# Kernel tuning notes

Measured on AMD Instinct MI355X. Metric: run time of the kernel, lower is better.

Reference implementation:

```python
import jax, jax.numpy as jnp
from jax import lax
import numpy as np

BATCH, SEQ, N, M, U = 256, 4096, 16, 8, 4  # batch, seq_len, state, obs, input dims


def setup_inputs() -> dict:
    key = jax.random.key(0)
    ks = jax.random.split(key, 8)
    # stable transition matrix (spectral radius < 1)
    A_raw = jax.random.normal(ks[0], (N, N), dtype=jnp.float32)
    A = 0.9 * A_raw / jnp.linalg.norm(A_raw, ord=2)
    B = jax.random.normal(ks[1], (N, U), dtype=jnp.float32) * 0.1
    C = jax.random.normal(ks[2], (M, N), dtype=jnp.float32) * 0.3
    # SPD noise covariances
    Q = 0.01 * jnp.eye(N, dtype=jnp.float32)
    R = 0.1 * jnp.eye(M, dtype=jnp.float32)
    obs = jax.random.normal(ks[3], (BATCH, SEQ, M), dtype=jnp.float32)
    inputs = jax.random.normal(ks[4], (BATCH, SEQ, U), dtype=jnp.float32)
    x0 = jax.random.normal(ks[5], (N,), dtype=jnp.float32)
    return {"obs": obs, "inputs": inputs, "A": A, "B": B, "C": C, "Q": Q, "R": R, "x0": x0}


def _kalman(obs, inputs, A, B, C, Q, R, x0):
    n = A.shape[0]
    bsz = obs.shape[0]
    eye_n = jnp.eye(n, dtype=obs.dtype)

    def step(carry, zu):
        x, P = carry              # x: (B, n), P: (n, n) shared across batch
        z, u = zu                 # z: (B, m), u: (B, u)
        # stage 1: state prediction
        x_pri = x @ A.T + u @ B.T               # (B, n)
        P_pri = A @ P @ A.T + Q                 # (n, n)
        # stage 2: measurement update
        S = C @ P_pri @ C.T + R                 # (m, m)
        K = P_pri @ C.T @ jnp.linalg.inv(S)     # (n, m)
        innov = z - x_pri @ C.T                 # (B, m)
        x_post = x_pri + innov @ K.T            # (B, n)
        P_post = (eye_n - K @ C) @ P_pri        # (n, n)
        return (x_post, P_post), x_post

    x_init = jnp.broadcast_to(x0, (bsz, n))
    zs = jnp.swapaxes(obs[:, 1:, :], 0, 1)      # (T-1, B, m)
    us = jnp.swapaxes(inputs[:, 1:, :], 0, 1)   # (T-1, B, u)
    _, xs = lax.scan(step, (x_init, eye_n), (zs, us))
    states = jnp.concatenate([x_init[:, None, :], jnp.swapaxes(xs, 0, 1)], axis=1)
    return states                                # (B, T, n)


def reference(obs, inputs, A, B, C, Q, R, x0):
    return _kalman(obs, inputs, A, B, C, Q, R, x0)
```

## Files before the change

### kernel.cpp

```cpp
#include <hip/hip_runtime.h>


#define SEQ_T  4096
#define NSTEP  4095
#define NB     256
#define NEX    8
#define LCH    32
#define NCHT   128

#define EX_OFF 0
#define ST_OFF (NEX*448)
#define HI_OFF (ST_OFF+448)
#define DB_OFF (HI_OFF+256)

template<int KQ>
__device__ __forceinline__ void bc4(const float* xr, float* xk) {
#pragma unroll
  for (int r = 0; r < 4; r++)
    xk[r] = __int_as_float(__builtin_amdgcn_update_dpp(
        0, __float_as_int(xr[r]), KQ * 0x55, 0xF, 0xF, true));
}

__global__ __launch_bounds__(64) void k_riccati(
    const float* __restrict__ Ag, const float* __restrict__ Bg,
    const float* __restrict__ Cg, const float* __restrict__ Qg,
    const float* __restrict__ Rg, float* __restrict__ ws)
{
  const int l = threadIdx.x;
  __shared__ float As[256], Qs[256], Cs[128], Bs[64], CA[128], CB[32];
  __shared__ float Pp[256], Vv[128], Km[128], Gm[256], T1[256], T2[256], Xs[64];

#pragma unroll
  for (int j=0;j<4;j++){ int e=l+64*j; As[e]=Ag[e]; Qs[e]=Qg[e]; }
  Cs[l]=Cg[l]; Cs[l+64]=Cg[l+64];
  Bs[l]=Bg[l];
  const float rr = Rg[l];
  __syncthreads();

  const int r4=l>>2, g4=l&3;
  const int r8=l>>3, c8=l&7;

  { int e=l; { int r=e>>4,c=e&15; float a=0.f;
      for (int k=0;k<16;k++) a+=Cs[r*16+k]*As[k*16+c]; CA[e]=a; }
    e=l+64; { int r=e>>4,c=e&15; float a=0.f;
      for (int k=0;k<16;k++) a+=Cs[r*16+k]*As[k*16+c]; CA[e]=a; }
    if (l<32){ int r=l>>2,c=l&3; float a=0.f;
      for (int k=0;k<16;k++) a+=Cs[r*16+k]*Bs[k*4+c]; CB[l]=a; }
#pragma unroll
    for (int j=0;j<4;j++){ int c=4*g4+j; float a=Qs[r4*16+c];
      for (int k=0;k<16;k++) a+=As[r4*16+k]*As[c*16+k]; Pp[r4*16+c]=a; }
  }
  __syncthreads();

  float kv0=0.f, kv1=0.f, bfv=0.f;
  for (int s=0;s<NEX;s++){
    { int e=l; { int r=e>>3,c=e&7; float a=0.f;
        for (int k=0;k<16;k++) a+=Pp[r*16+k]*Cs[c*16+k]; Vv[e]=a; }
      e=l+64; { int r=e>>3,c=e&7; float a=0.f;
        for (int k=0;k<16;k++) a+=Pp[r*16+k]*Cs[c*16+k]; Vv[e]=a; } }
    __syncthreads();
    { float sv=rr;
      for (int k=0;k<16;k++) sv += Cs[r8*16+k]*Vv[k*8+c8];
      float xv = (r8==c8)?1.f:0.f;
#pragma unroll
      for (int p=0;p<8;p++){
        float spp = __shfl(sv, p*9);
        float pr  = 1.0f/spp;
        float spc = __shfl(sv, p*8+c8);
        float xpc = __shfl(xv, p*8+c8);
        float srp = __shfl(sv, r8*8+p);
        float f = srp*pr;
        if (r8==p){ sv = spc*pr; xv = xpc*pr; }
        else      { sv -= f*spc; xv -= f*xpc; }
      }
      Xs[l]=xv; }
    __syncthreads();
    { int e=l; { int r=e>>3,c=e&7; float a=0.f;
        for (int k=0;k<8;k++) a+=Vv[r*8+k]*Xs[k*8+c]; kv0=a; Km[e]=a; }
      e=l+64; { int r=e>>3,c=e&7; float a=0.f;
        for (int k=0;k<8;k++) a+=Vv[r*8+k]*Xs[k*8+c]; kv1=a; Km[e]=a; } }
    __syncthreads();
    { float gv[4];
#pragma unroll
      for (int j=0;j<4;j++){ int c=4*g4+j;
        float a=As[r4*16+c], w=Pp[r4*16+c];
        for (int k=0;k<8;k++){ a -= Km[r4*8+k]*CA[k*16+c]; w -= Km[r4*8+k]*Vv[c*8+k]; }
        gv[j]=a; Gm[r4*16+c]=a; Pp[r4*16+c]=w; }
      bfv = Bs[l];
      for (int k=0;k<8;k++) bfv -= Km[r4*8+k]*CB[k*4+g4];
      float* dst = ws + EX_OFF + s*448;
      *reinterpret_cast<float4*>(dst + r4*16 + g4*4) =
          make_float4(gv[0],gv[1],gv[2],gv[3]);
      dst[256+l]=kv0; dst[256+64+l]=kv1; dst[384+l]=bfv;
    }
    __syncthreads();
#pragma unroll
    for (int j=0;j<4;j++){ int c=4*g4+j; float a=0.f;
      for (int k=0;k<16;k++) a+=As[r4*16+k]*Pp[k*16+c]; T1[r4*16+c]=a; }
    __syncthreads();
#pragma unroll
    for (int j=0;j<4;j++){ int c=4*g4+j; float a=Qs[r4*16+c];
      for (int k=0;k<16;k++) a+=T1[r4*16+k]*As[c*16+k]; Pp[r4*16+c]=a; }
    __syncthreads();
  }
  { float* dst = ws + ST_OFF;
    *reinterpret_cast<float4*>(dst + r4*16 + g4*4) =
        *reinterpret_cast<float4*>(&Gm[r4*16 + g4*4]);
    dst[256+l]=kv0; dst[256+64+l]=kv1; dst[384+l]=bfv; }
#pragma unroll
  for (int j=0;j<4;j++) T1[l+64*j]=Gm[l+64*j];
  __syncthreads();
  for (int it=0; it<5; it++){
#pragma unroll
    for (int j=0;j<4;j++){ int c=4*g4+j; float a=0.f;
      for (int k=0;k<16;k++) a+=T1[r4*16+k]*T1[k*16+c]; T2[r4*16+c]=a; }
    __syncthreads();
#pragma unroll
    for (int j=0;j<4;j++) T1[l+64*j]=T2[l+64*j];
    __syncthreads();
  }
#pragma unroll
  for (int j=0;j<4;j++) ws[HI_OFF + l+64*j] = T1[l+64*j];
}

__device__ __forceinline__ void ld_rows(const float* __restrict__ m, int q,
    float gm[4][16], float km[4][8], float bf[4][4]) {
#pragma unroll
  for (int r=0;r<4;r++){
    const int row = 4*q + r;
    const float4* gp = reinterpret_cast<const float4*>(m + row*16);
#pragma unroll
    for (int kk=0;kk<4;kk++){ float4 t=gp[kk];
      gm[r][4*kk]=t.x; gm[r][4*kk+1]=t.y; gm[r][4*kk+2]=t.z; gm[r][4*kk+3]=t.w; }
    const float4* kp = reinterpret_cast<const float4*>(m + 256 + row*8);
#pragma unroll
    for (int kk=0;kk<2;kk++){ float4 t=kp[kk];
      km[r][4*kk]=t.x; km[r][4*kk+1]=t.y; km[r][4*kk+2]=t.z; km[r][4*kk+3]=t.w; }
    float4 t = *reinterpret_cast<const float4*>(m + 384 + row*4);
    bf[r][0]=t.x; bf[r][1]=t.y; bf[r][2]=t.z; bf[r][3]=t.w;
  }
}

template<int MODE>
__device__ __forceinline__ void chunk_run(
    const float* __restrict__ obs, const float* __restrict__ inp,
    const float* __restrict__ x0g, float* __restrict__ ws,
    float* __restrict__ out, int j, int g)
{
  const int l=threadIdx.x, bl=l>>2, q=l&3, b=g*16+bl;
  const int s0 = j*LCH;
  const int nst = (NSTEP - s0 < LCH) ? (NSTEP - s0) : LCH;

  float gm[4][16], km[4][8], bf[4][4];
  if (MODE==1) ld_rows(ws + EX_OFF, q, gm, km, bf);
  else         ld_rows(ws + ST_OFF, q, gm, km, bf);

  float xr[4];
  if (MODE==0){ xr[0]=xr[1]=xr[2]=xr[3]=0.f; }
  else if (MODE==1){
    float4 x = *reinterpret_cast<const float4*>(x0g + q*4);
    xr[0]=x.x; xr[1]=x.y; xr[2]=x.z; xr[3]=x.w;
    *reinterpret_cast<float4*>(out + (size_t)b*(SEQ_T*16) + q*4) = x;
  } else {
    float4 x = *reinterpret_cast<const float4*>(
        ws + DB_OFF + (size_t)(j-1)*(NB*16) + b*16 + q*4);
    xr[0]=x.x; xr[1]=x.y; xr[2]=x.z; xr[3]=x.w;
  }

  const float* zp = obs + (size_t)b*(SEQ_T*8);
  const float* up = inp + (size_t)b*(SEQ_T*4);

  float4 z0a = *reinterpret_cast<const float4*>(zp + (size_t)(s0+1)*8);
  float4 z1a = *reinterpret_cast<const float4*>(zp + (size_t)(s0+1)*8 + 4);
  float4 u0a = *reinterpret_cast<const float4*>(up + (size_t)(s0+1)*4);
  float4 z0b = *reinterpret_cast<const float4*>(zp + (size_t)(s0+2)*8);
  float4 z1b = *reinterpret_cast<const float4*>(zp + (size_t)(s0+2)*8 + 4);
  float4 u0b = *reinterpret_cast<const float4*>(up + (size_t)(s0+2)*4);

  for (int st=0; st<nst; st++){
    float4 z0=z0a, z1=z1a, u0=u0a;
    z0a=z0b; z1a=z1b; u0a=u0b;
    { int tn = s0+st+3; tn = (tn > NSTEP) ? NSTEP : tn;
      const size_t t = (size_t)tn;
      z0b = *reinterpret_cast<const float4*>(zp + t*8);
      z1b = *reinterpret_cast<const float4*>(zp + t*8 + 4);
      u0b = *reinterpret_cast<const float4*>(up + t*4);
    }
    float xk[16];
    bc4<0>(xr, xk); bc4<1>(xr, xk+4); bc4<2>(xr, xk+8); bc4<3>(xr, xk+12);
    float xn[4];
#pragma unroll
    for (int r=0;r<4;r++){
      float a = bf[r][0]*u0.x + bf[r][1]*u0.y + bf[r][2]*u0.z + bf[r][3]*u0.w;
      a += km[r][0]*z0.x + km[r][1]*z0.y + km[r][2]*z0.z + km[r][3]*z0.w;
      a += km[r][4]*z1.x + km[r][5]*z1.y + km[r][6]*z1.z + km[r][7]*z1.w;
#pragma unroll
      for (int k=0;k<16;k++) a += gm[r][k]*xk[k];
      xn[r]=a;
    }
#pragma unroll
    for (int r=0;r<4;r++) xr[r]=xn[r];
    if (MODE>=1)
      *reinterpret_cast<float4*>(out + (size_t)b*(SEQ_T*16) +
                                 (size_t)(s0+st+1)*16 + q*4) =
          make_float4(xr[0],xr[1],xr[2],xr[3]);
    if (MODE==1 && st+1 < nst){
      if (st+1 < NEX)       ld_rows(ws + EX_OFF + (st+1)*448, q, gm, km, bf);
      else if (st+1 == NEX) ld_rows(ws + ST_OFF, q, gm, km, bf);
    }
  }
  if (MODE<=1)
    *reinterpret_cast<float4*>(ws + DB_OFF + (size_t)j*(NB*16) + b*16 + q*4) =
        make_float4(xr[0],xr[1],xr[2],xr[3]);
}

__global__ __launch_bounds__(64,2) void k_phase1(
    const float* __restrict__ obs, const float* __restrict__ inp,
    const float* __restrict__ x0g, float* __restrict__ ws,
    float* __restrict__ out)
{
  const int j = blockIdx.x>>4, g = blockIdx.x&15;
  if (j==0) chunk_run<1>(obs, inp, x0g, ws, out, j, g);
  else      chunk_run<0>(obs, inp, x0g, ws, out, j, g);
}

__global__ __launch_bounds__(64,2) void k_phase3(
    const float* __restrict__ obs, const float* __restrict__ inp,
    float* __restrict__ ws, float* __restrict__ out)
{
  const int j = 1 + (blockIdx.x>>4), g = blockIdx.x&15;
  chunk_run<2>(obs, inp, nullptr, ws, out, j, g);
}

__global__ __launch_bounds__(256) void k_scan(float* __restrict__ ws)
{
  const int tid=threadIdx.x, lane=tid&63, wv=tid>>6, bl=lane>>2, q=lane&3;
  const int b = blockIdx.x*64 + wv*16 + bl;
  float hm[4][16];
#pragma unroll
  for (int r=0;r<4;r++){
    const int row = 4*q + r;
    const float4* hp = reinterpret_cast<const float4*>(ws + HI_OFF + row*16);
#pragma unroll
    for (int kk=0;kk<4;kk++){ float4 t=hp[kk];
      hm[r][4*kk]=t.x; hm[r][4*kk+1]=t.y; hm[r][4*kk+2]=t.z; hm[r][4*kk+3]=t.w; }
  }
  float* p = ws + DB_OFF + (size_t)b*16 + q*4;
  float4 xi = *reinterpret_cast<const float4*>(p);
  float xr[4]={xi.x,xi.y,xi.z,xi.w};

  float4 dbuf[14];
#pragma unroll
  for (int k=0;k<14;k++)
    dbuf[k] = *reinterpret_cast<const float4*>(p + (size_t)(1+k)*(NB*16));

  for (int base=0; base<9; base++){
#pragma unroll
    for (int k=0;k<14;k++){
      const int jj = 1 + base*14 + k;
      float4 d = dbuf[k];
      if (jj+14 <= 126)
        dbuf[k] = *reinterpret_cast<const float4*>(
            p + (size_t)(jj+14)*(NB*16));
      float xk[16];
      bc4<0>(xr, xk); bc4<1>(xr, xk+4); bc4<2>(xr, xk+8); bc4<3>(xr, xk+12);
      float xn[4]={d.x,d.y,d.z,d.w};
#pragma unroll
      for (int r=0;r<4;r++){
#pragma unroll
        for (int kk=0;kk<16;kk++) xn[r]+=hm[r][kk]*xk[kk];
      }
#pragma unroll
      for (int r=0;r<4;r++) xr[r]=xn[r];
      *reinterpret_cast<float4*>(p + (size_t)jj*(NB*16)) =
          make_float4(xr[0],xr[1],xr[2],xr[3]);
    }
  }
}

extern "C" void kernel_launch(void* const* d_in, const int* in_sizes, int n_in,
                              void* d_out, int out_size, void* d_ws, size_t ws_size,
                              hipStream_t stream) {
  const float* obs = (const float*)d_in[0];
  const float* inp = (const float*)d_in[1];
  const float* A   = (const float*)d_in[2];
  const float* B   = (const float*)d_in[3];
  const float* C   = (const float*)d_in[4];
  const float* Q   = (const float*)d_in[5];
  const float* R   = (const float*)d_in[6];
  const float* x0  = (const float*)d_in[7];
  float* out = (float*)d_out;
  float* ws  = (float*)d_ws;

  k_riccati<<<dim3(1),        dim3(64),  0, stream>>>(A, B, C, Q, R, ws);
  k_phase1 <<<dim3(NCHT*16),  dim3(64),  0, stream>>>(obs, inp, x0, ws, out);
  k_scan   <<<dim3(4),        dim3(256), 0, stream>>>(ws);
  k_phase3 <<<dim3(127*16),   dim3(64),  0, stream>>>(obs, inp, ws, out);
}
```

Before: 196.5 us.

## Replace phase-3 recurrence rerun with linear correction using precomputed G powers

Phase 1 now writes the zero-start chunk states for every chunk to the output. The Riccati kernel precomputes the powers G^1..G^32 into the workspace. Phase 3 no longer re-reads obs/inputs or reruns the sequential recurrence. Each step instead adds G^(i+1) times the carried-in chunk-start state to the stored output, which removes the serial dependency. In exchange, phase 1 writes all outputs that phase 3 must read back, and the Riccati kernel runs 31 serial matmuls instead of 5.

```diff
diff --git a/kernel.cpp b/kernel.cpp
--- a/kernel.cpp
+++ b/kernel.cpp
@@ -12,6 +12,7 @@
 #define ST_OFF (NEX*448)
 #define HI_OFF (ST_OFF+448)
 #define DB_OFF (HI_OFF+256)
+#define GP_OFF (DB_OFF + NCHT*(NB*16))
 
 template<int KQ>
 __device__ __forceinline__ void bc4(const float* xr, float* xk) {
@@ -110,17 +111,22 @@
 #pragma unroll
   for (int j=0;j<4;j++) T1[l+64*j]=Gm[l+64*j];
   __syncthreads();
-  for (int it=0; it<5; it++){
+  for (int it=0; it<32; it++){
+#pragma unroll
+    for (int j=0;j<4;j++) ws[GP_OFF + it*256 + l+64*j] = T1[l+64*j];
+    if (it==31){
+#pragma unroll
+      for (int j=0;j<4;j++) ws[HI_OFF + l+64*j] = T1[l+64*j];
+      break;
+    }
 #pragma unroll
     for (int j=0;j<4;j++){ int c=4*g4+j; float a=0.f;
-      for (int k=0;k<16;k++) a+=T1[r4*16+k]*T1[k*16+c]; T2[r4*16+c]=a; }
+      for (int k=0;k<16;k++) a+=T1[r4*16+k]*Gm[k*16+c]; T2[r4*16+c]=a; }
     __syncthreads();
 #pragma unroll
     for (int j=0;j<4;j++) T1[l+64*j]=T2[l+64*j];
     __syncthreads();
   }
-#pragma unroll
-  for (int j=0;j<4;j++) ws[HI_OFF + l+64*j] = T1[l+64*j];
 }
 
 __device__ __forceinline__ void ld_rows(const float* __restrict__ m, int q,
@@ -157,14 +163,10 @@
 
   float xr[4];
   if (MODE==0){ xr[0]=xr[1]=xr[2]=xr[3]=0.f; }
-  else if (MODE==1){
+  else {
     float4 x = *reinterpret_cast<const float4*>(x0g + q*4);
     xr[0]=x.x; xr[1]=x.y; xr[2]=x.z; xr[3]=x.w;
     *reinterpret_cast<float4*>(out + (size_t)b*(SEQ_T*16) + q*4) = x;
-  } else {
-    float4 x = *reinterpret_cast<const float4*>(
-        ws + DB_OFF + (size_t)(j-1)*(NB*16) + b*16 + q*4);
-    xr[0]=x.x; xr[1]=x.y; xr[2]=x.z; xr[3]=x.w;
   }
 
   const float* zp = obs + (size_t)b*(SEQ_T*8);
@@ -200,18 +202,16 @@
     }
 #pragma unroll
     for (int r=0;r<4;r++) xr[r]=xn[r];
-    if (MODE>=1)
-      *reinterpret_cast<float4*>(out + (size_t)b*(SEQ_T*16) +
-                                 (size_t)(s0+st+1)*16 + q*4) =
-          make_float4(xr[0],xr[1],xr[2],xr[3]);
+    *reinterpret_cast<float4*>(out + (size_t)b*(SEQ_T*16) +
+                               (size_t)(s0+st+1)*16 + q*4) =
+        make_float4(xr[0],xr[1],xr[2],xr[3]);
     if (MODE==1 && st+1 < nst){
       if (st+1 < NEX)       ld_rows(ws + EX_OFF + (st+1)*448, q, gm, km, bf);
       else if (st+1 == NEX) ld_rows(ws + ST_OFF, q, gm, km, bf);
     }
   }
-  if (MODE<=1)
-    *reinterpret_cast<float4*>(ws + DB_OFF + (size_t)j*(NB*16) + b*16 + q*4) =
-        make_float4(xr[0],xr[1],xr[2],xr[3]);
+  *reinterpret_cast<float4*>(ws + DB_OFF + (size_t)j*(NB*16) + b*16 + q*4) =
+      make_float4(xr[0],xr[1],xr[2],xr[3]);
 }
 
 __global__ __launch_bounds__(64,2) void k_phase1(
@@ -224,12 +224,40 @@
   else      chunk_run<0>(obs, inp, x0g, ws, out, j, g);
 }
 
-__global__ __launch_bounds__(64,2) void k_phase3(
-    const float* __restrict__ obs, const float* __restrict__ inp,
+__global__ __launch_bounds__(64,2) void k_corr(
     float* __restrict__ ws, float* __restrict__ out)
 {
   const int j = 1 + (blockIdx.x>>4), g = blockIdx.x&15;
-  chunk_run<2>(obs, inp, nullptr, ws, out, j, g);
+  const int l = threadIdx.x, bl=l>>2, q=l&3, b=g*16+bl;
+  const int s0 = j*LCH;
+  const int nst = (NSTEP - s0 < LCH) ? (NSTEP - s0) : LCH;
+
+  float xr[4];
+  { float4 x = *reinterpret_cast<const float4*>(
+      ws + DB_OFF + (size_t)(j-1)*(NB*16) + b*16 + q*4);
+    xr[0]=x.x; xr[1]=x.y; xr[2]=x.z; xr[3]=x.w; }
+  float xk[16];
+  bc4<0>(xr, xk); bc4<1>(xr, xk+4); bc4<2>(xr, xk+8); bc4<3>(xr, xk+12);
+
+  float* yp = out + (size_t)b*(SEQ_T*16) + (size_t)(s0+1)*16 + q*4;
+  const float* gpw = ws + GP_OFF + q*64;
+
+  for (int i=0; i<nst; i++){
+    const float* pm = gpw + i*256;
+    float4 y = *reinterpret_cast<const float4*>(yp + (size_t)i*16);
+    float xn[4];
+#pragma unroll
+    for (int r=0;r<4;r++){
+      const float4* pr = reinterpret_cast<const float4*>(pm + r*16);
+      float4 p0=pr[0], p1=pr[1], p2=pr[2], p3=pr[3];
+      xn[r] = p0.x*xk[0]+p0.y*xk[1]+p0.z*xk[2]+p0.w*xk[3]
+            + p1.x*xk[4]+p1.y*xk[5]+p1.z*xk[6]+p1.w*xk[7]
+            + p2.x*xk[8]+p2.y*xk[9]+p2.z*xk[10]+p2.w*xk[11]
+            + p3.x*xk[12]+p3.y*xk[13]+p3.z*xk[14]+p3.w*xk[15];
+    }
+    *reinterpret_cast<float4*>(yp + (size_t)i*16) =
+        make_float4(y.x+xn[0], y.y+xn[1], y.z+xn[2], y.w+xn[3]);
+  }
 }
 
 __global__ __launch_bounds__(256) void k_scan(float* __restrict__ ws)
@@ -295,5 +323,5 @@
   k_riccati<<<dim3(1),        dim3(64),  0, stream>>>(A, B, C, Q, R, ws);
   k_phase1 <<<dim3(NCHT*16),  dim3(64),  0, stream>>>(obs, inp, x0, ws, out);
   k_scan   <<<dim3(4),        dim3(256), 0, stream>>>(ws);
-  k_phase3 <<<dim3(127*16),   dim3(64),  0, stream>>>(obs, inp, ws, out);
-}
+  k_corr   <<<dim3(127*16),   dim3(64),  0, stream>>>(ws, out);
+}
```

Result: slower. 323.0 us (+64.4%).
